# Performance work log

Hardware: AMD Instinct MI355X
Metric: run time of the kernel (lower is better)

## Reference

```python
import jax, jax.numpy as jnp
import numpy as np

N_NODES = 100_000
N_EDGES = 3_200_000
N_FEAT = 128
N_HID = 8
N_CLASSES = 10


def setup_inputs() -> dict:
    key = jax.random.key(0)
    ks = jax.random.split(key, 16)
    g = lambda k, shape, fan_in: jax.random.normal(k, shape, jnp.float32) / np.sqrt(fan_in)
    inp = {}
    inp['x'] = jax.random.normal(ks[0], (N_NODES, N_FEAT), jnp.float32)
    inp['edge_index'] = jax.random.randint(ks[1], (2, N_EDGES), 0, N_NODES, jnp.int32)
    # lin: Linear(F, 8)
    inp['lin_w'] = g(ks[2], (N_FEAT, N_HID), N_FEAT)
    inp['lin_b'] = jnp.zeros((N_HID,), jnp.float32)
    # conv1: GATConv(8, 8, heads=2)
    inp['w1'] = g(ks[3], (N_HID, 2 * N_HID), N_HID)
    inp['a1_src'] = g(ks[4], (2, N_HID), N_HID)
    inp['a1_dst'] = g(ks[5], (2, N_HID), N_HID)
    inp['b1'] = jnp.zeros((2 * N_HID,), jnp.float32)
    # conv2: GATConv(16, 8, heads=2)
    inp['w2'] = g(ks[6], (2 * N_HID, 2 * N_HID), 2 * N_HID)
    inp['a2_src'] = g(ks[7], (2, N_HID), N_HID)
    inp['a2_dst'] = g(ks[8], (2, N_HID), N_HID)
    inp['b2'] = jnp.zeros((2 * N_HID,), jnp.float32)
    # conv3: GATConv(16, num_classes, heads=1, concat=False)
    inp['w3'] = g(ks[9], (2 * N_HID, N_CLASSES), 2 * N_HID)
    inp['a3_src'] = g(ks[10], (1, N_CLASSES), N_CLASSES)
    inp['a3_dst'] = g(ks[11], (1, N_CLASSES), N_CLASSES)
    inp['b3'] = jnp.zeros((N_CLASSES,), jnp.float32)
    return inp


def _gat_conv(x, W, a_src, a_dst, b, src, dst, heads, out_c, concat):
    """PyG GATConv with pre-appended self-loops in (src, dst)."""
    N = x.shape[0]
    xl = (x @ W).reshape(N, heads, out_c)                 # [N,H,C]
    alpha_src = (xl * a_src[None]).sum(-1)                # [N,H]
    alpha_dst = (xl * a_dst[None]).sum(-1)                # [N,H]
    e = jax.nn.leaky_relu(alpha_src[src] + alpha_dst[dst], 0.2)  # [E,H]
    # segment softmax over destination nodes
    m = jax.ops.segment_max(e, dst, num_segments=N)
    e = jnp.exp(e - m[dst])
    s = jax.ops.segment_sum(e, dst, num_segments=N)
    alpha = e / s[dst]                                    # [E,H]
    msg = xl[src] * alpha[:, :, None]                     # [E,H,C]
    out = jax.ops.segment_sum(msg, dst, num_segments=N)   # [N,H,C]
    out = out.reshape(N, heads * out_c) if concat else out.mean(axis=1)
    return out + b


def reference(x, edge_index, lin_w, lin_b, w1, a1_src, a1_dst, b1,
              w2, a2_src, a2_dst, b2, w3, a3_src, a3_dst, b3):
    N = x.shape[0]
    loops = jnp.arange(N, dtype=edge_index.dtype)
    src = jnp.concatenate([edge_index[0], loops])
    dst = jnp.concatenate([edge_index[1], loops])
    lrelu = lambda v: jax.nn.leaky_relu(v, 0.01)
    h = lrelu(x @ lin_w + lin_b)
    h = lrelu(_gat_conv(h, w1, a1_src, a1_dst, b1, src, dst, 2, N_HID, True))
    h = lrelu(_gat_conv(h, w2, a2_src, a2_dst, b2, src, dst, 2, N_HID, True))
    h = _gat_conv(h, w3, a3_src, a3_dst, b3, src, dst, 1, N_CLASSES, False)
    return jax.nn.log_softmax(h, axis=-1)
```

## Files before the change

kernel.cpp:

```cpp
#include <hip/hip_runtime.h>
#include <hip/hip_fp16.h>
#include <math.h>

#define N_NODES 100000
#define N_EDGES 3200000
#define ET (N_EDGES + N_NODES)
#define SLOT 80
#define KMAX 5
#define SHIFT 8
#define BNODES 256
#define NBUCK 391
#define BCAP 9088
#define P1_T 1024
#define E_PER 8
#define P1_WG ((N_EDGES + P1_T * E_PER - 1) / (P1_T * E_PER))
#define BUILD_T 1024
#define SCAN_T 1024
#define SCAN_CHUNK 98
#define LOG2E 1.44269504088896f

typedef _Float16 h2 __attribute__((ext_vector_type(2)));

__device__ __forceinline__ float lrelu(float v, float s) { return v > 0.f ? v : v * s; }
__device__ __forceinline__ float fexp2(float x) { return __builtin_amdgcn_exp2f(x); }

__device__ __forceinline__ h2 f2h2(float f) {
    union { float f; h2 h; } u; u.f = f; return u.h;
}

__device__ __forceinline__ float fdot2(h2 a, h2 b, float c) {
#if __has_builtin(__builtin_amdgcn_fdot2)
    return __builtin_amdgcn_fdot2(a, b, c, false);
#else
    return c + (float)a.x * (float)b.x + (float)a.y * (float)b.y;
#endif
}

template <int CTRL>
__device__ __forceinline__ float dppmov(float v) {
    return __int_as_float(__builtin_amdgcn_update_dpp(0, __float_as_int(v), CTRL, 0xF, 0xF, true));
}

__device__ __forceinline__ void reduce8(float a[8], float& ssum, int lane) {
    int b0 = lane & 1, b1 = (lane >> 1) & 1, b2 = (lane >> 2) & 1;
    float q0 = (b0 ? a[4] : a[0]) + dppmov<0xB1>(b0 ? a[0] : a[4]);
    float q1 = (b0 ? a[5] : a[1]) + dppmov<0xB1>(b0 ? a[1] : a[5]);
    float q2 = (b0 ? a[6] : a[2]) + dppmov<0xB1>(b0 ? a[2] : a[6]);
    float q3 = (b0 ? a[7] : a[3]) + dppmov<0xB1>(b0 ? a[3] : a[7]);
    float r0 = (b1 ? q2 : q0) + dppmov<0x4E>(b1 ? q0 : q2);
    float r1 = (b1 ? q3 : q1) + dppmov<0x4E>(b1 ? q1 : q3);
    float t  = (b2 ? r1 : r0) + __shfl_xor(b2 ? r0 : r1, 4, 64);
    t += __shfl_xor(t, 8, 64);
    a[0] = t;
    ssum += dppmov<0xB1>(ssum);
    ssum += dppmov<0x4E>(ssum);
    ssum += __shfl_xor(ssum, 4, 64);
    ssum += __shfl_xor(ssum, 8, 64);
}

__global__ void __launch_bounds__(P1_T) part_kernel(const int* __restrict__ ei,
                                                    int* __restrict__ bcur,
                                                    unsigned* __restrict__ pairs) {
    __shared__ int hist[NBUCK];
    __shared__ int gbase[NBUCK];
    int t = threadIdx.x;
    for (int i = t; i < NBUCK; i += P1_T) hist[i] = 0;
    __syncthreads();
    int base = blockIdx.x * (P1_T * E_PER);
    int s[E_PER], d[E_PER], r[E_PER];
#pragma unroll
    for (int k = 0; k < E_PER; k++) {
        int e = base + k * P1_T + t;
        if (e < N_EDGES) {
            s[k] = ei[e];
            d[k] = ei[N_EDGES + e];
            r[k] = atomicAdd(&hist[d[k] >> SHIFT], 1);
        }
    }
    __syncthreads();
    for (int i = t; i < NBUCK; i += P1_T)
        gbase[i] = (hist[i] > 0) ? atomicAdd(&bcur[i], hist[i]) : 0;
    __syncthreads();
#pragma unroll
    for (int k = 0; k < E_PER; k++) {
        int e = base + k * P1_T + t;
        if (e < N_EDGES) {
            int b = d[k] >> SHIFT;
            int pos = gbase[b] + r[k];
            if (pos < BCAP)
                pairs[(size_t)b * BCAP + pos] =
                    ((unsigned)(d[k] & (BNODES - 1)) << 17) | (unsigned)s[k];
        }
    }
}

__global__ void __launch_bounds__(BUILD_T) build_kernel(const int* __restrict__ bcur,
                                                        const unsigned* __restrict__ pairs,
                                                        int* __restrict__ csr,
                                                        int* __restrict__ deg) {
    __shared__ int offs[BNODES];
    int b = blockIdx.x;
    int t = threadIdx.x;
    int node0 = b << SHIFT;
    if (t < BNODES) {
        int n = node0 + t;
        if (n < N_NODES) {
            csr[n * SLOT] = n;
            offs[t] = 1;
        } else offs[t] = 0;
    }
    __syncthreads();
    int cnt = min(bcur[b], BCAP);
    for (int i = t; i < cnt; i += BUILD_T) {
        unsigned v = pairs[(size_t)b * BCAP + i];
        int ln = v >> 17;
        int s = v & 0x1FFFF;
        int pos = atomicAdd(&offs[ln], 1);
        if (pos < SLOT) csr[(node0 + ln) * SLOT + pos] = s;
    }
    __syncthreads();
    if (t < BNODES) {
        int n = node0 + t;
        if (n < N_NODES) deg[n] = offs[t];
    }
}

__global__ void count_kernel(const int* __restrict__ ei, int* __restrict__ deg) {
    int e = blockIdx.x * blockDim.x + threadIdx.x;
    if (e >= ET) return;
    int d = (e < N_EDGES) ? ei[N_EDGES + e] : (e - N_EDGES);
    atomicAdd(&deg[d], 1);
}

__global__ void scan_kernel(const int* __restrict__ deg, int* __restrict__ rowptr,
                            int* __restrict__ cursor) {
    __shared__ int sums[SCAN_T];
    int t = threadIdx.x;
    int start = t * SCAN_CHUNK;
    int end = min(start + SCAN_CHUNK, N_NODES);
    int s = 0;
    for (int i = start; i < end; i++) s += deg[i];
    sums[t] = s;
    __syncthreads();
    for (int off = 1; off < SCAN_T; off <<= 1) {
        int v = sums[t];
        int add = (t >= off) ? sums[t - off] : 0;
        __syncthreads();
        sums[t] = v + add;
        __syncthreads();
    }
    int base = (t > 0) ? sums[t - 1] : 0;
    for (int i = start; i < end; i++) {
        rowptr[i] = base;
        cursor[i] = base;
        base += deg[i];
    }
    if (t == SCAN_T - 1) rowptr[N_NODES] = base;
}

__global__ void scatter_kernel(const int* __restrict__ ei, int* __restrict__ cursor,
                               int* __restrict__ csr) {
    int e = blockIdx.x * blockDim.x + threadIdx.x;
    if (e >= ET) return;
    int s, d;
    if (e < N_EDGES) { s = ei[e]; d = ei[N_EDGES + e]; } else { s = d = e - N_EDGES; }
    int pos = atomicAdd(&cursor[d], 1);
    csr[pos] = s;
}

template <int CIN, int H, int C, int XLS>
__global__ void prep_kernel(const float* __restrict__ hin, const float* __restrict__ W,
                            const float* __restrict__ a_src, const float* __restrict__ a_dst,
                            __half* __restrict__ xl, float* __restrict__ asrc,
                            float* __restrict__ adst) {
    __shared__ float Ws[CIN * H * C];
    __shared__ float As[H * C];
    __shared__ float Ad[H * C];
    for (int i = threadIdx.x; i < CIN * H * C; i += blockDim.x) Ws[i] = W[i];
    for (int i = threadIdx.x; i < H * C; i += blockDim.x) {
        As[i] = a_src[i] * LOG2E;
        Ad[i] = a_dst[i] * LOG2E;
    }
    __syncthreads();
    int n = blockIdx.x * blockDim.x + threadIdx.x;
    if (n >= N_NODES) return;
    float hreg[CIN];
#pragma unroll
    for (int i = 0; i < CIN; i += 4) {
        float4 v = *(const float4*)&hin[n * CIN + i];
        hreg[i] = v.x; hreg[i + 1] = v.y; hreg[i + 2] = v.z; hreg[i + 3] = v.w;
    }
#pragma unroll
    for (int h = 0; h < H; h++) {
        float as = 0.f, ad = 0.f;
#pragma unroll
        for (int c = 0; c < C; c++) {
            float v = 0.f;
#pragma unroll
            for (int i = 0; i < CIN; i++) v += hreg[i] * Ws[i * H * C + h * C + c];
            xl[n * XLS + h * C + c] = __float2half_rn(v);
            as += v * As[h * C + c];
            ad += v * Ad[h * C + c];
        }
        asrc[n * H + h] = as;
        adst[n * H + h] = ad;
    }
#pragma unroll
    for (int c = H * C; c < XLS; c++) xl[n * XLS + c] = __float2half_rn(0.f);
}

template <int H, int C, int XLS>
__global__ __launch_bounds__(256) void prep_lin_kernel(
        const float* __restrict__ x, const float* __restrict__ lw, const float* __restrict__ lb,
        const float* __restrict__ W, const float* __restrict__ a_src,
        const float* __restrict__ a_dst, __half* __restrict__ xl,
        float* __restrict__ asrc, float* __restrict__ adst) {
    __shared__ float LW[128 * 8];
    __shared__ float Ws[8 * H * C];
    __shared__ float As[H * C];
    __shared__ float Ad[H * C];
    __shared__ float Lb[8];
    for (int i = threadIdx.x; i < 128 * 8; i += 256) LW[i] = lw[i];
    for (int i = threadIdx.x; i < 8 * H * C; i += 256) Ws[i] = W[i];
    for (int i = threadIdx.x; i < H * C; i += 256) {
        As[i] = a_src[i] * LOG2E;
        Ad[i] = a_dst[i] * LOG2E;
    }
    if (threadIdx.x < 8) Lb[threadIdx.x] = lb[threadIdx.x];
    __syncthreads();
    int n = blockIdx.x * blockDim.x + threadIdx.x;
    if (n >= N_NODES) return;
    float hreg[8];
#pragma unroll
    for (int c = 0; c < 8; c++) hreg[c] = 0.f;
#pragma unroll 8
    for (int i = 0; i < 128; i += 4) {
        float4 v = *(const float4*)&x[n * 128 + i];
#pragma unroll
        for (int c = 0; c < 8; c++) hreg[c] += v.x * LW[(i + 0) * 8 + c];
#pragma unroll
        for (int c = 0; c < 8; c++) hreg[c] += v.y * LW[(i + 1) * 8 + c];
#pragma unroll
        for (int c = 0; c < 8; c++) hreg[c] += v.z * LW[(i + 2) * 8 + c];
#pragma unroll
        for (int c = 0; c < 8; c++) hreg[c] += v.w * LW[(i + 3) * 8 + c];
    }
#pragma unroll
    for (int c = 0; c < 8; c++) hreg[c] = lrelu(hreg[c] + Lb[c], 0.01f);
#pragma unroll
    for (int h = 0; h < H; h++) {
        float as = 0.f, ad = 0.f;
#pragma unroll
        for (int c = 0; c < C; c++) {
            float v = 0.f;
#pragma unroll
            for (int i = 0; i < 8; i++) v += hreg[i] * Ws[i * H * C + h * C + c];
            xl[n * XLS + h * C + c] = __float2half_rn(v);
            as += v * As[h * C + c];
            ad += v * Ad[h * C + c];
        }
        asrc[n * H + h] = as;
        adst[n * H + h] = ad;
    }
#pragma unroll
    for (int c = H * C; c < XLS; c++) xl[n * XLS + c] = __float2half_rn(0.f);
}

__global__ __launch_bounds__(256) void gat64_h2(const int* __restrict__ cnt_,
                                                const int* __restrict__ csr,
                                                const float* __restrict__ a_src,
                                                const float* __restrict__ adst,
                                                const __half* __restrict__ xl,
                                                const float* __restrict__ b,
                                                float* __restrict__ hout) {
    int wg = blockIdx.x * 4 + (threadIdx.x >> 6);
    int lane = threadIdx.x & 63;
    int eg = lane & 15;
    int q  = (lane >> 4) & 1;
    int nd = lane >> 5;
    int n = wg * 2 + nd;
    float4 as0 = *(const float4*)&a_src[q * 8];
    float4 as1 = *(const float4*)&a_src[q * 8 + 4];
    h2 av0 = {(_Float16)(as0.x * LOG2E), (_Float16)(as0.y * LOG2E)};
    h2 av1 = {(_Float16)(as0.z * LOG2E), (_Float16)(as0.w * LOG2E)};
    h2 av2 = {(_Float16)(as1.x * LOG2E), (_Float16)(as1.y * LOG2E)};
    h2 av3 = {(_Float16)(as1.z * LOG2E), (_Float16)(as1.w * LOG2E)};
    int cnt = min(cnt_[n], SLOT);
    float ad = adst[n * 2 + q];
    int idx[KMAX];
#pragma unroll
    for (int k = 0; k < KMAX; k++) {
        int i = eg + (k << 4);
        idx[k] = (i < cnt) ? csr[n * SLOT + i] : -1;
    }
    float ssum = 0.f;
    float a[8] = {0.f, 0.f, 0.f, 0.f, 0.f, 0.f, 0.f, 0.f};
#pragma unroll
    for (int k = 0; k < KMAX; k++) {
        int s = idx[k];
        if (s >= 0) {
            float4 raw = *(const float4*)&xl[s * 16 + q * 8];
            h2 x0 = f2h2(raw.x), x1 = f2h2(raw.y), x2 = f2h2(raw.z), x3 = f2h2(raw.w);
            float e = fdot2(x0, av0, fdot2(x1, av1, fdot2(x2, av2, fdot2(x3, av3, ad))));
            float w = fexp2(fmaxf(e, 0.2f * e));
            ssum += w;
            a[0] += w * (float)x0.x; a[1] += w * (float)x0.y;
            a[2] += w * (float)x1.x; a[3] += w * (float)x1.y;
            a[4] += w * (float)x2.x; a[5] += w * (float)x2.y;
            a[6] += w * (float)x3.x; a[7] += w * (float)x3.y;
        }
    }
    reduce8(a, ssum, lane);
    if ((lane & 8) == 0) {
        int ch = 8 * q + 4 * (lane & 1) + 2 * ((lane >> 1) & 1) + ((lane >> 2) & 1);
        hout[n * 16 + ch] = lrelu(a[0] / ssum + b[ch], 0.01f);
    }
}

__global__ __launch_bounds__(256) void gat64_ls(const int* __restrict__ cnt_,
                                                const int* __restrict__ csr,
                                                const float* __restrict__ a_src,
                                                const float* __restrict__ adst,
                                                const __half* __restrict__ xl,
                                                const float* __restrict__ b,
                                                float* __restrict__ out) {
    int wg = blockIdx.x * 4 + (threadIdx.x >> 6);
    int lane = threadIdx.x & 63;
    int eg = lane & 15;
    int q  = (lane >> 4) & 1;
    int nd = lane >> 5;
    int n = wg * 2 + nd;
    float avf[8];
#pragma unroll
    for (int j = 0; j < 8; j++) {
        int c = q * 8 + j;
        avf[j] = (c < 10) ? a_src[c] * LOG2E : 0.f;
    }
    h2 av0 = {(_Float16)avf[0], (_Float16)avf[1]};
    h2 av1 = {(_Float16)avf[2], (_Float16)avf[3]};
    h2 av2 = {(_Float16)avf[4], (_Float16)avf[5]};
    h2 av3 = {(_Float16)avf[6], (_Float16)avf[7]};
    int cnt = min(cnt_[n], SLOT);
    float adh = adst[n] * 0.5f;
    int idx[KMAX];
#pragma unroll
    for (int k = 0; k < KMAX; k++) {
        int i = eg + (k << 4);
        idx[k] = (i < cnt) ? csr[n * SLOT + i] : -1;
    }
    float ssum = 0.f;
    float a[8] = {0.f, 0.f, 0.f, 0.f, 0.f, 0.f, 0.f, 0.f};
#pragma unroll
    for (int k = 0; k < KMAX; k++) {
        int s = idx[k];
        if (s >= 0) {
            float4 raw = *(const float4*)&xl[s * 16 + q * 8];
            h2 x0 = f2h2(raw.x), x1 = f2h2(raw.y), x2 = f2h2(raw.z), x3 = f2h2(raw.w);
            float part = fdot2(x0, av0, fdot2(x1, av1, fdot2(x2, av2, fdot2(x3, av3, adh))));
            float e = part + __shfl_xor(part, 16, 64);
            float w = fexp2(fmaxf(e, 0.2f * e));
            ssum += w;
            a[0] += w * (float)x0.x; a[1] += w * (float)x0.y;
            a[2] += w * (float)x1.x; a[3] += w * (float)x1.y;
            a[4] += w * (float)x2.x; a[5] += w * (float)x2.y;
            a[6] += w * (float)x3.x; a[7] += w * (float)x3.y;
        }
    }
    reduce8(a, ssum, lane);
    int ch = 8 * q + 4 * (lane & 1) + 2 * ((lane >> 1) & 1) + ((lane >> 2) & 1);
    float u = (ch < 10) ? a[0] / ssum + b[ch] : -INFINITY;
    float m = u;
    m = fmaxf(m, dppmov<0xB1>(m));
    m = fmaxf(m, dppmov<0x4E>(m));
    m = fmaxf(m, __shfl_xor(m, 4, 64));
    m = fmaxf(m, __shfl_xor(m, 8, 64));
    m = fmaxf(m, __shfl_xor(m, 16, 64));
    float ex = (ch < 10 && (lane & 8) == 0) ? __expf(u - m) : 0.f;
    ex += dppmov<0xB1>(ex);
    ex += dppmov<0x4E>(ex);
    ex += __shfl_xor(ex, 4, 64);
    ex += __shfl_xor(ex, 8, 64);
    ex += __shfl_xor(ex, 16, 64);
    float lse = m + __logf(ex);
    if ((lane & 8) == 0 && ch < 10) out[n * 10 + ch] = u - lse;
}

__global__ void gat16_h2(const int* __restrict__ rowptr, const int* __restrict__ csr,
                         const float* __restrict__ asrc, const float* __restrict__ adst,
                         const __half* __restrict__ xl, const float* __restrict__ b,
                         float* __restrict__ hout) {
    int tid = blockIdx.x * blockDim.x + threadIdx.x;
    int wave = tid >> 6;
    int lane = threadIdx.x & 63;
    int g = lane >> 4;
    int c = lane & 15;
    int h = c >> 3;
    int n = wave * 4 + g;
    if (n >= N_NODES) return;
    int beg = rowptr[n], cnt = rowptr[n + 1] - beg;
    float adn = adst[n * 2 + h];
    float ssum = 0.f, pa = 0.f;
#pragma unroll 4
    for (int i = 0; i < cnt; i++) {
        int s = csr[beg + i];
        float e = asrc[s * 2 + h] + adn;
        float w = fexp2(fmaxf(e, 0.2f * e));
        ssum += w;
        pa += w * __half2float(xl[s * 16 + c]);
    }
    hout[n * 16 + c] = lrelu(pa / ssum + b[c], 0.01f);
}

__global__ void gat16_ls(const int* __restrict__ rowptr, const int* __restrict__ csr,
                         const float* __restrict__ asrc, const float* __restrict__ adst,
                         const __half* __restrict__ xl, const float* __restrict__ b,
                         float* __restrict__ out) {
    int tid = blockIdx.x * blockDim.x + threadIdx.x;
    int wave = tid >> 6;
    int lane = threadIdx.x & 63;
    int g = lane >> 4;
    int c = lane & 15;
    int n = wave * 4 + g;
    if (n >= N_NODES) return;
    int beg = rowptr[n], cnt = rowptr[n + 1] - beg;
    float adn = adst[n];
    float ssum = 0.f, pa = 0.f;
#pragma unroll 4
    for (int i = 0; i < cnt; i++) {
        int s = csr[beg + i];
        float e = asrc[s] + adn;
        float w = fexp2(fmaxf(e, 0.2f * e));
        ssum += w;
        pa += w * __half2float(xl[s * 16 + c]);
    }
    float v = pa / ssum + ((c < 10) ? b[c] : 0.f);
    float vm = (c < 10) ? v : -INFINITY;
#pragma unroll
    for (int off = 8; off >= 1; off >>= 1) vm = fmaxf(vm, __shfl_xor(vm, off, 16));
    float ex = (c < 10) ? __expf(v - vm) : 0.f;
    float sum = ex;
#pragma unroll
    for (int off = 8; off >= 1; off >>= 1) sum += __shfl_xor(sum, off, 16);
    float lse = vm + __logf(sum);
    if (c < 10) out[n * 10 + c] = v - lse;
}

extern "C" void kernel_launch(void* const* d_in, const int* in_sizes, int n_in,
                              void* d_out, int out_size, void* d_ws, size_t ws_size,
                              hipStream_t stream) {
    const float* x     = (const float*)d_in[0];
    const int*   ei    = (const int*)d_in[1];
    const float* lin_w = (const float*)d_in[2];
    const float* lin_b = (const float*)d_in[3];
    const float* w1    = (const float*)d_in[4];
    const float* a1s   = (const float*)d_in[5];
    const float* a1d   = (const float*)d_in[6];
    const float* b1    = (const float*)d_in[7];
    const float* w2    = (const float*)d_in[8];
    const float* a2s   = (const float*)d_in[9];
    const float* a2d   = (const float*)d_in[10];
    const float* b2    = (const float*)d_in[11];
    const float* w3    = (const float*)d_in[12];
    const float* a3s   = (const float*)d_in[13];
    const float* a3d   = (const float*)d_in[14];
    const float* b3    = (const float*)d_in[15];

    float* ws = (float*)d_ws;
    float* slotH  = ws;
    __half* slotX = (__half*)(ws + 1600000);
    float* as_    = ws + 3200000;
    float* ad_    = ws + 3400000;
    unsigned* pairs = (unsigned*)ws;
    int* csrP = (int*)(ws + 3600000);
    int* degP = (int*)(ws + 3600000 + N_NODES * SLOT);
    int* bcur = degP + N_NODES;
    size_t need_new = (size_t)(3600000 + N_NODES * SLOT + N_NODES + 512) * 4;

    int use_bucket = (ws_size >= need_new) ? 1 : 0;

    int* degC    = (int*)(ws + 3600000);
    int* rowptrC = degC + N_NODES;
    int* cursorC = rowptrC + N_NODES + 1;
    int* csrC    = cursorC + N_NODES;

    dim3 B(256);
    int nb_n  = (N_NODES + 255) / 256;
    int nb_et = (ET + 255) / 256;
    int nb_g  = (N_NODES + 15) / 16;
    int nb_w2 = N_NODES / 8;

    if (use_bucket) {
        hipMemsetAsync(bcur, 0, 512 * sizeof(int), stream);
        part_kernel<<<P1_WG, P1_T, 0, stream>>>(ei, bcur, pairs);
        build_kernel<<<NBUCK, BUILD_T, 0, stream>>>(bcur, pairs, csrP, degP);
    } else {
        hipMemsetAsync(degC, 0, N_NODES * sizeof(int), stream);
        count_kernel<<<nb_et, B, 0, stream>>>(ei, degC);
        scan_kernel<<<1, SCAN_T, 0, stream>>>(degC, rowptrC, cursorC);
        scatter_kernel<<<nb_et, B, 0, stream>>>(ei, cursorC, csrC);
    }

    prep_lin_kernel<2, 8, 16><<<nb_n, B, 0, stream>>>(x, lin_w, lin_b, w1, a1s, a1d,
                                                      slotX, as_, ad_);
    if (use_bucket) gat64_h2<<<nb_w2, B, 0, stream>>>(degP, csrP, a1s, ad_, slotX, b1, slotH);
    else            gat16_h2<<<nb_g, B, 0, stream>>>(rowptrC, csrC, as_, ad_, slotX, b1, slotH);

    prep_kernel<16, 2, 8, 16><<<nb_n, B, 0, stream>>>(slotH, w2, a2s, a2d, slotX, as_, ad_);
    if (use_bucket) gat64_h2<<<nb_w2, B, 0, stream>>>(degP, csrP, a2s, ad_, slotX, b2, slotH);
    else            gat16_h2<<<nb_g, B, 0, stream>>>(rowptrC, csrC, as_, ad_, slotX, b2, slotH);

    prep_kernel<16, 1, 10, 16><<<nb_n, B, 0, stream>>>(slotH, w3, a3s, a3d, slotX, as_, ad_);
    if (use_bucket) gat64_ls<<<nb_w2, B, 0, stream>>>(degP, csrP, a3s, ad_, slotX, b3, (float*)d_out);
    else            gat16_ls<<<nb_g, B, 0, stream>>>(rowptrC, csrC, as_, ad_, slotX, b3, (float*)d_out);
}
```

Baseline: 278.7 us.

## Replace global bucket atomics with per-block local partition and start offsets

The partition kernel no longer reserves space in fixed-capacity global buckets through global atomics. Each block now does a shared-memory prefix scan over its bucket histogram, writes its edges contiguously within its own chunk, and records per-bucket start offsets. The build kernel then has each wavefront walk the per-block segments for its bucket. This removes the memset, the global atomic contention and the BCAP overflow truncation, at the cost of a 9-step scan in every partition block and a second strided read pattern of many small segments in the build kernel.

```diff
diff --git a/kernel.cpp b/kernel.cpp
--- a/kernel.cpp
+++ b/kernel.cpp
@@ -10,7 +10,6 @@
 #define SHIFT 8
 #define BNODES 256
 #define NBUCK 391
-#define BCAP 9088
 #define P1_T 1024
 #define E_PER 8
 #define P1_WG ((N_EDGES + P1_T * E_PER - 1) / (P1_T * E_PER))
@@ -59,10 +58,10 @@
 }
 
 __global__ void __launch_bounds__(P1_T) part_kernel(const int* __restrict__ ei,
-                                                    int* __restrict__ bcur,
+                                                    int* __restrict__ starts,
                                                     unsigned* __restrict__ pairs) {
     __shared__ int hist[NBUCK];
-    __shared__ int gbase[NBUCK];
+    __shared__ int scan[512];
     int t = threadIdx.x;
     for (int i = t; i < NBUCK; i += P1_T) hist[i] = 0;
     __syncthreads();
@@ -78,23 +77,28 @@
         }
     }
     __syncthreads();
-    for (int i = t; i < NBUCK; i += P1_T)
-        gbase[i] = (hist[i] > 0) ? atomicAdd(&bcur[i], hist[i]) : 0;
-    __syncthreads();
+    if (t < 512) scan[t] = (t < NBUCK) ? hist[t] : 0;
+    __syncthreads();
+    for (int off = 1; off < 512; off <<= 1) {
+        int v = 0, add = 0;
+        if (t < 512) { v = scan[t]; if (t >= off) add = scan[t - off]; }
+        __syncthreads();
+        if (t < 512) scan[t] = v + add;
+        __syncthreads();
+    }
+    if (t <= NBUCK) starts[blockIdx.x * (NBUCK + 1) + t] = base + (t ? scan[t - 1] : 0);
 #pragma unroll
     for (int k = 0; k < E_PER; k++) {
         int e = base + k * P1_T + t;
         if (e < N_EDGES) {
             int b = d[k] >> SHIFT;
-            int pos = gbase[b] + r[k];
-            if (pos < BCAP)
-                pairs[(size_t)b * BCAP + pos] =
-                    ((unsigned)(d[k] & (BNODES - 1)) << 17) | (unsigned)s[k];
-        }
-    }
-}
-
-__global__ void __launch_bounds__(BUILD_T) build_kernel(const int* __restrict__ bcur,
+            int pos = (b ? scan[b - 1] : 0) + r[k];
+            pairs[base + pos] = ((unsigned)(d[k] & (BNODES - 1)) << 17) | (unsigned)s[k];
+        }
+    }
+}
+
+__global__ void __launch_bounds__(BUILD_T) build_kernel(const int* __restrict__ starts,
                                                         const unsigned* __restrict__ pairs,
                                                         int* __restrict__ csr,
                                                         int* __restrict__ deg) {
@@ -110,13 +114,17 @@
         } else offs[t] = 0;
     }
     __syncthreads();
-    int cnt = min(bcur[b], BCAP);
-    for (int i = t; i < cnt; i += BUILD_T) {
-        unsigned v = pairs[(size_t)b * BCAP + i];
-        int ln = v >> 17;
-        int s = v & 0x1FFFF;
-        int pos = atomicAdd(&offs[ln], 1);
-        if (pos < SLOT) csr[(node0 + ln) * SLOT + pos] = s;
+    int wid = t >> 6, lane = t & 63;
+    for (int B = wid; B < P1_WG; B += (BUILD_T / 64)) {
+        int st = starts[B * (NBUCK + 1) + b];
+        int en = starts[B * (NBUCK + 1) + b + 1];
+        for (int i = st + lane; i < en; i += 64) {
+            unsigned v = pairs[i];
+            int ln = v >> 17;
+            int sc = v & 0x1FFFF;
+            int pos = atomicAdd(&offs[ln], 1);
+            if (pos < SLOT) csr[(node0 + ln) * SLOT + pos] = sc;
+        }
     }
     __syncthreads();
     if (t < BNODES) {
@@ -472,9 +480,10 @@
     float* ad_    = ws + 3400000;
     unsigned* pairs = (unsigned*)ws;
     int* csrP = (int*)(ws + 3600000);
-    int* degP = (int*)(ws + 3600000 + N_NODES * SLOT);
-    int* bcur = degP + N_NODES;
-    size_t need_new = (size_t)(3600000 + N_NODES * SLOT + N_NODES + 512) * 4;
+    int* degP = csrP + (size_t)N_NODES * SLOT;
+    int* startsP = degP + N_NODES;
+    size_t need_new = (size_t)(3600000 + (size_t)N_NODES * SLOT + N_NODES
+                               + (size_t)P1_WG * (NBUCK + 1) + 64) * 4;
 
     int use_bucket = (ws_size >= need_new) ? 1 : 0;
 
@@ -490,9 +499,8 @@
     int nb_w2 = N_NODES / 8;
 
     if (use_bucket) {
-        hipMemsetAsync(bcur, 0, 512 * sizeof(int), stream);
-        part_kernel<<<P1_WG, P1_T, 0, stream>>>(ei, bcur, pairs);
-        build_kernel<<<NBUCK, BUILD_T, 0, stream>>>(bcur, pairs, csrP, degP);
+        part_kernel<<<P1_WG, P1_T, 0, stream>>>(ei, startsP, pairs);
+        build_kernel<<<NBUCK, BUILD_T, 0, stream>>>(startsP, pairs, csrP, degP);
     } else {
         hipMemsetAsync(degC, 0, N_NODES * sizeof(int), stream);
         count_kernel<<<nb_et, B, 0, stream>>>(ei, degC);
```

New measurement: 280.2 us. No clear change (+0.5%).
